# Kernel optimization log

Hardware: AMD Instinct MI355X
Metric: run time of the kernel (lower is better)

## Reference

```python
import jax, jax.numpy as jnp
import numpy as np

EPS = 1e-5

def rmsnorm(x):
    # BitLinear pre-norm (no learnable scale), per BitNet b1.58 reference impl
    return x * jax.lax.rsqrt(jnp.mean(x * x, axis=-1, keepdims=True) + EPS)

def act_quant(x):
    # per-token absmax 8-bit quantization with straight-through estimator
    scale = 127.0 / jnp.clip(jnp.max(jnp.abs(x), axis=-1, keepdims=True), 1e-5)
    q = jnp.clip(jnp.round(x * scale), -128.0, 127.0) / scale
    return x + jax.lax.stop_gradient(q - x)

def weight_quant(w):
    # absmean ternary quantization {-1,0,1} with STE
    scale = 1.0 / jnp.clip(jnp.mean(jnp.abs(w)), 1e-5)
    q = jnp.clip(jnp.round(w * scale), -1.0, 1.0) / scale
    return w + jax.lax.stop_gradient(q - w)

def bitlinear(x, w, b):
    # x: [b, s, d_in], w: [d_out, d_in] (torch Linear layout), b: [d_out]
    xq = act_quant(rmsnorm(x))
    wq = weight_quant(w)
    return jnp.einsum('bsd,fd->bsf', xq, wq) + b

def setup_inputs() -> dict:
    key = jax.random.key(0)
    k0, k1, k2 = jax.random.split(key, 3)
    B, S, D, F = 2, 8192, 1024, 4096  # inner_dim = dim * mult = 4096
    x = jax.random.normal(k0, (B, S, D), dtype=jnp.float32)
    w1 = jax.random.normal(k1, (F, D), dtype=jnp.float32) * (1.0 / np.sqrt(D))
    b1 = jnp.zeros((F,), dtype=jnp.float32)
    w2 = jax.random.normal(k2, (D, F), dtype=jnp.float32) * (1.0 / np.sqrt(F))
    b2 = jnp.zeros((D,), dtype=jnp.float32)
    return {"x": x, "w1": w1, "b1": b1, "w2": w2, "b2": b2}

def reference(x, w1, b1, w2, b2):
    h = bitlinear(x, w1, b1)
    h = jax.nn.gelu(h, approximate=False)  # nn.GELU() default is exact
    # post_act_ln=False -> no LayerNorm; dropout p=0.0 -> identity
    return bitlinear(h, w2, b2)
```

## Files before the change

### kernel.cpp

```cpp
#include <hip/hip_runtime.h>
#include <hip/hip_bf16.h>
#include <stdint.h>

typedef int i32x4 __attribute__((ext_vector_type(4)));

__device__ __forceinline__ float blo(unsigned int u) {
  unsigned int v = u << 16; float f; __builtin_memcpy(&f, &v, 4); return f;
}
__device__ __forceinline__ float bhi(unsigned int u) {
  unsigned int v = u & 0xffff0000u; float f; __builtin_memcpy(&f, &v, 4); return f;
}
__device__ __forceinline__ int pack4q(float a, float b, float c, float d, float qm) {
  int i0 = (int)rintf(a * qm) & 255;
  int i1 = (int)rintf(b * qm) & 255;
  int i2 = (int)rintf(c * qm) & 255;
  int i3 = (int)rintf(d * qm) & 255;
  return i0 | (i1 << 8) | (i2 << 16) | (i3 << 24);
}

__device__ __forceinline__ float fast_gelu(float v) {
  float u = v * 0.70710678118654752f;
  float s = fabsf(u);
  float den = fmaf(0.3275911f, s, 1.0f);
  float t;
  asm("v_rcp_f32 %0, %1" : "=v"(t) : "v"(den));
  float p = t * fmaf(t, fmaf(t, fmaf(t, fmaf(t, 1.061405429f, -1.453152027f),
                                     1.421413741f), -0.284496736f), 0.254829592f);
  float e = fmaf(-p, __expf(-u * u), 1.0f);
  float er = copysignf(e, u);
  return 0.5f * v * (1.0f + er);
}

__global__ void k_reduce_abs2(const float* __restrict__ w1, const float* __restrict__ w2,
                              long n4, float* __restrict__ partials) {
  const int half = gridDim.x >> 1;
  const float* w = (blockIdx.x < half) ? w1 : w2;
  int b = (blockIdx.x < half) ? blockIdx.x : blockIdx.x - half;
  const float4* wv = (const float4*)w;
  float s = 0.0f;
  long stride = (long)half * blockDim.x;
  for (long i = (long)b * blockDim.x + threadIdx.x; i < n4; i += stride) {
    float4 v = wv[i];
    s += fabsf(v.x) + fabsf(v.y) + fabsf(v.z) + fabsf(v.w);
  }
  #pragma unroll
  for (int off = 32; off; off >>= 1) s += __shfl_down(s, off);
  __shared__ float sw[4];
  if ((threadIdx.x & 63) == 0) sw[threadIdx.x >> 6] = s;
  __syncthreads();
  if (threadIdx.x == 0) partials[blockIdx.x] = sw[0] + sw[1] + sw[2] + sw[3];
}

__global__ void k_finalize_scales(const float* __restrict__ p1, const float* __restrict__ p2,
                                  float* __restrict__ scales, float inv1, float inv2) {
  int t = threadIdx.x;
  float s1 = p1[t], s2 = p2[t];
  #pragma unroll
  for (int off = 32; off; off >>= 1) { s1 += __shfl_down(s1, off); s2 += __shfl_down(s2, off); }
  __shared__ float a1[4], a2[4];
  if ((t & 63) == 0) { a1[t >> 6] = s1; a2[t >> 6] = s2; }
  __syncthreads();
  if (t == 0) {
    scales[0] = fmaxf((a1[0]+a1[1]+a1[2]+a1[3]) * inv1, 1e-5f);
    scales[1] = fmaxf((a2[0]+a2[1]+a2[2]+a2[3]) * inv2, 1e-5f);
  }
}

__global__ void k_quant_w2(const float* __restrict__ w1, char* __restrict__ wq1,
                           const float* __restrict__ w2, char* __restrict__ wq2,
                           long n4, const float* __restrict__ scales) {
  const int half = gridDim.x >> 1;
  const bool first = blockIdx.x < half;
  const float* w = first ? w1 : w2;
  char* wq = first ? wq1 : wq2;
  int b = first ? blockIdx.x : blockIdx.x - half;
  float s = 1.0f / scales[first ? 0 : 1];
  const float4* wv = (const float4*)w;
  int* qv = (int*)wq;
  long stride = (long)half * blockDim.x;
  for (long i = (long)b * blockDim.x + threadIdx.x; i < n4; i += stride) {
    float4 v = wv[i];
    int b0 = (int)fminf(fmaxf(rintf(v.x * s), -1.0f), 1.0f) & 255;
    int b1 = (int)fminf(fmaxf(rintf(v.y * s), -1.0f), 1.0f) & 255;
    int b2 = (int)fminf(fmaxf(rintf(v.z * s), -1.0f), 1.0f) & 255;
    int b3 = (int)fminf(fmaxf(rintf(v.w * s), -1.0f), 1.0f) & 255;
    qv[i] = b0 | (b1 << 8) | (b2 << 16) | (b3 << 24);
  }
}

__global__ void k_actq_x(const float* __restrict__ x, char* __restrict__ xq,
                         float* __restrict__ alpha) {
  const int D = 1024;
  size_t t = blockIdx.x;
  int tid = threadIdx.x;
  const float4* row = (const float4*)(x + t * (size_t)D);
  float4 v = row[tid];
  float ss = v.x*v.x + v.y*v.y + v.z*v.z + v.w*v.w;
  float am = fmaxf(fmaxf(fabsf(v.x), fabsf(v.y)), fmaxf(fabsf(v.z), fabsf(v.w)));
  #pragma unroll
  for (int off = 32; off; off >>= 1) {
    ss += __shfl_down(ss, off);
    am = fmaxf(am, __shfl_down(am, off));
  }
  __shared__ float s_ss[4], s_am[4];
  if ((tid & 63) == 0) { s_ss[tid >> 6] = ss; s_am[tid >> 6] = am; }
  __syncthreads();
  ss = s_ss[0] + s_ss[1] + s_ss[2] + s_ss[3];
  am = fmaxf(fmaxf(s_am[0], s_am[1]), fmaxf(s_am[2], s_am[3]));
  float rms = rsqrtf(ss * (1.0f / D) + 1e-5f);
  float a   = fmaxf(am * rms, 1e-5f);
  float qs  = 127.0f / a;
  if (tid == 0) alpha[t] = a * (1.0f / 127.0f);
  int b0 = (int)fminf(fmaxf(rintf((v.x * rms) * qs), -128.0f), 127.0f) & 255;
  int b1 = (int)fminf(fmaxf(rintf((v.y * rms) * qs), -128.0f), 127.0f) & 255;
  int b2 = (int)fminf(fmaxf(rintf((v.z * rms) * qs), -128.0f), 127.0f) & 255;
  int b3 = (int)fminf(fmaxf(rintf((v.w * rms) * qs), -128.0f), 127.0f) & 255;
  ((int*)xq)[t * 256 + tid] = b0 | (b1 << 8) | (b2 << 16) | (b3 << 24);
}

__global__ void k_actq_h(__hip_bfloat16* __restrict__ h, float* __restrict__ alpha) {
  const int F = 4096;
  size_t t = blockIdx.x;
  int tid = threadIdx.x;
  char* rb = (char*)(h + t * (size_t)F);
  const uint4* row = (const uint4*)rb;
  uint4 u0 = row[tid], u1 = row[tid + 256];
  unsigned int uu[8] = {u0.x, u0.y, u0.z, u0.w, u1.x, u1.y, u1.z, u1.w};
  float ss = 0.0f, am = 0.0f;
  #pragma unroll
  for (int i = 0; i < 8; i++) {
    float f0 = blo(uu[i]), f1 = bhi(uu[i]);
    ss += f0 * f0 + f1 * f1;
    am = fmaxf(am, fmaxf(fabsf(f0), fabsf(f1)));
  }
  #pragma unroll
  for (int off = 32; off; off >>= 1) {
    ss += __shfl_down(ss, off);
    am = fmaxf(am, __shfl_down(am, off));
  }
  __shared__ float s_ss[4], s_am[4];
  if ((tid & 63) == 0) { s_ss[tid >> 6] = ss; s_am[tid >> 6] = am; }
  __syncthreads();
  ss = s_ss[0] + s_ss[1] + s_ss[2] + s_ss[3];
  am = fmaxf(fmaxf(s_am[0], s_am[1]), fmaxf(s_am[2], s_am[3]));
  float rms = rsqrtf(ss * (1.0f / F) + 1e-5f);
  float a   = fmaxf(am * rms, 1e-5f);
  float qm  = rms * (127.0f / a);
  if (tid == 0) alpha[t] = a * (1.0f / 127.0f);
  uint2 w0, w1;
  w0.x = (unsigned)pack4q(blo(uu[0]), bhi(uu[0]), blo(uu[1]), bhi(uu[1]), qm);
  w0.y = (unsigned)pack4q(blo(uu[2]), bhi(uu[2]), blo(uu[3]), bhi(uu[3]), qm);
  w1.x = (unsigned)pack4q(blo(uu[4]), bhi(uu[4]), blo(uu[5]), bhi(uu[5]), qm);
  w1.y = (unsigned)pack4q(blo(uu[6]), bhi(uu[6]), blo(uu[7]), bhi(uu[7]), qm);
  *(uint2*)(rb + 8 * tid) = w0;
  *(uint2*)(rb + 2048 + 8 * tid) = w1;
}

#define GLD16(GP, LP) __builtin_amdgcn_global_load_lds( \
    (__attribute__((address_space(1))) void*)(GP), \
    (__attribute__((address_space(3))) void*)(LP), 16, 0, 0)
#define VMCNT3 asm volatile("s_waitcnt vmcnt(3)" ::: "memory")
#define VMCNT0 asm volatile("s_waitcnt vmcnt(0)" ::: "memory")
#define LGKM0  do { asm volatile("s_waitcnt lgkmcnt(0)" ::: "memory"); __builtin_amdgcn_sched_barrier(0); } while(0)

template<int EPI>
__global__ __launch_bounds__(512, 4) void k_gemm_i8(
    const char* __restrict__ A, int lda,
    const char* __restrict__ B,
    const float* __restrict__ bias, const float* __restrict__ alpha,
    const float* __restrict__ scales, int which,
    void* __restrict__ Cout, int N, int K, int lgnbx)
{
  __shared__ __align__(16) char lA[3 * 8192];
  __shared__ __align__(16) char lB[3 * 16384];
  const int tid = threadIdx.x, lane = tid & 63, wid = tid >> 6;
  const int wm = wid >> 2, wn = wid & 3;
  const int nwg = gridDim.x, bid = blockIdx.x;
  const int swz = (bid & 7) * (nwg >> 3) + (bid >> 3);
  const int bx = swz & ((1 << lgnbx) - 1), by = swz >> lgnbx;
  const int m0 = by * 128, n0 = bx * 256;
  const int NT = K >> 6;

  const int srow = tid >> 2, slot = tid & 3;
  const int sswz = (slot ^ ((srow >> 1) & 3)) * 16;
  const char* gA0 = A + (size_t)(m0 +       srow) * lda + sswz;
  const char* gB0 = B + (size_t)(n0 +       srow) * K   + sswz;
  const char* gB1 = B + (size_t)(n0 + 128 + srow) * K   + sswz;
  const int ldst = srow * 64 + slot * 16;

  const int lr = lane & 15;
  const int kx = ((lane >> 4) ^ ((lane >> 1) & 3)) * 16;
  const int aoff = (wm * 64 + lr) * 64 + kx;
  const int boff = (wn * 64 + lr) * 64 + kx;

  GLD16(gA0,      lA + ldst);
  GLD16(gB0,      lB + ldst);
  GLD16(gB1,      lB + 8192 + ldst);
  GLD16(gA0 + 64, lA + 8192 + ldst);
  GLD16(gB0 + 64, lB + 16384 + ldst);
  GLD16(gB1 + 64, lB + 16384 + 8192 + ldst);

  i32x4 acc[4][4] = {};
  int cur = 0, nx1 = 1, nx2 = 2;
  for (int t = 0; t < NT; ++t) {
    if (t + 1 < NT) { VMCNT3; } else { VMCNT0; }
    __builtin_amdgcn_s_barrier();
    if (t + 2 < NT) {
      GLD16(gA0 + 64 * (t + 2), lA + nx2 * 8192 + ldst);
      GLD16(gB0 + 64 * (t + 2), lB + nx2 * 16384 + ldst);
      GLD16(gB1 + 64 * (t + 2), lB + nx2 * 16384 + 8192 + ldst);
    }
    i32x4 av[4], bv[4];
    {
      const char* pa = lA + cur * 8192 + aoff;
      const char* pb = lB + cur * 16384 + boff;
      #pragma unroll
      for (int j = 0; j < 4; ++j) av[j] = *(const i32x4*)(pa + j * 1024);
      #pragma unroll
      for (int n = 0; n < 4; ++n) bv[n] = *(const i32x4*)(pb + n * 1024);
    }
    LGKM0;
    __builtin_amdgcn_s_setprio(1);
    #pragma unroll
    for (int j = 0; j < 4; ++j)
      #pragma unroll
      for (int n = 0; n < 4; ++n)
        acc[j][n] = __builtin_amdgcn_mfma_i32_16x16x64_i8(av[j], bv[n], acc[j][n], 0, 0, 0);
    __builtin_amdgcn_s_setprio(0);
    int tmp = cur; cur = nx1; nx1 = nx2; nx2 = tmp;
  }

  const float wdq = scales[which];
  const int lq4 = (lane >> 4) * 4;
  #pragma unroll
  for (int m = 0; m < 4; ++m) {
    const int rowb = m0 + wm * 64 + m * 16 + lq4;
    float al[4];
    #pragma unroll
    for (int q = 0; q < 4; ++q) al[q] = alpha[rowb + q] * wdq;
    #pragma unroll
    for (int n = 0; n < 4; ++n) {
      const int col = n0 + wn * 64 + n * 16 + lr;
      const float bb = bias[col];
      #pragma unroll
      for (int q = 0; q < 4; ++q) {
        float v = (float)acc[m][n][q] * al[q] + bb;
        if constexpr (EPI == 0) {
          ((__hip_bfloat16*)Cout)[(size_t)(rowb + q) * N + col] = __float2bfloat16(fast_gelu(v));
        } else {
          ((float*)Cout)[(size_t)(rowb + q) * N + col] = v;
        }
      }
    }
  }
}

extern "C" void kernel_launch(void* const* d_in, const int* in_sizes, int n_in,
                              void* d_out, int out_size, void* d_ws, size_t ws_size,
                              hipStream_t stream) {
  const float* x  = (const float*)d_in[0];
  const float* w1 = (const float*)d_in[1];
  const float* b1 = (const float*)d_in[2];
  const float* w2 = (const float*)d_in[3];
  const float* b2 = (const float*)d_in[4];
  const int  F = in_sizes[2];
  const int  D = in_sizes[4];
  const long T = (long)in_sizes[0] / D;
  const long nW = (long)F * D;

  char* ws = (char*)d_ws;
  float* partials = (float*)ws;
  float* scales   = partials + 512;
  float* alpha1 = (float*)(ws + 4096);
  float* alpha2 = alpha1 + T;
  size_t off = 4096 + 2 * (size_t)T * sizeof(float);
  off = (off + 255) & ~(size_t)255;
  char* w1q = ws + off; off += (size_t)nW;
  char* w2q = ws + off; off += (size_t)nW;
  char* xq  = ws + off; off += (size_t)T * D;
  off = (off + 255) & ~(size_t)255;
  __hip_bfloat16* h = (__hip_bfloat16*)(ws + off); off += (size_t)T * F * 2;
  if (ws_size < off) return;

  float invW = (float)(1.0 / (double)nW);
  k_reduce_abs2<<<512, 256, 0, stream>>>(w1, w2, nW / 4, partials);
  k_finalize_scales<<<1, 256, 0, stream>>>(partials, partials + 256, scales, invW, invW);
  k_quant_w2<<<4096, 256, 0, stream>>>(w1, w1q, w2, w2q, nW / 4, scales);
  k_actq_x<<<(unsigned)T, 256, 0, stream>>>(x, xq, alpha1);

  dim3 g1((unsigned)((T / 128) * (F / 256)));
  k_gemm_i8<0><<<g1, 512, 0, stream>>>(xq, D, w1q, b1, alpha1, scales, 0,
                                       h, F, D, __builtin_ctz(F / 256));

  k_actq_h<<<(unsigned)T, 256, 0, stream>>>(h, alpha2);

  dim3 g2((unsigned)((T / 128) * (D / 256)));
  k_gemm_i8<1><<<g2, 512, 0, stream>>>((const char*)h, F * 2, w2q, b2, alpha2, scales, 1,
                                       (float*)d_out, D, F, __builtin_ctz(D / 256));
}
```

Baseline: 244.4 us.

## Use 4-wave GEMM blocks with 64x128 per-wave tiles

The int8 GEMM block shrinks from 512 to 256 threads (4 waves in a 2x2 grid) while keeping the 128x256 block tile. Each wave now computes a 64x128 subtile with 32 accumulators, and each thread issues six global-to-LDS loads per stage instead of three, with the wait count adjusted to match. The aim is more MFMA work per LDS read and fewer waves contending for the barrier. In exchange it raises VGPR pressure and lowers occupancy (launch bounds go to 256 threads with 2 blocks per SM).

Result: slower. 257.7 us (+5.4%).

```diff
diff --git a/kernel.cpp b/kernel.cpp
--- a/kernel.cpp
+++ b/kernel.cpp
@@ -159,12 +159,12 @@
 #define GLD16(GP, LP) __builtin_amdgcn_global_load_lds( \
     (__attribute__((address_space(1))) void*)(GP), \
     (__attribute__((address_space(3))) void*)(LP), 16, 0, 0)
-#define VMCNT3 asm volatile("s_waitcnt vmcnt(3)" ::: "memory")
+#define VMCNT6 asm volatile("s_waitcnt vmcnt(6)" ::: "memory")
 #define VMCNT0 asm volatile("s_waitcnt vmcnt(0)" ::: "memory")
 #define LGKM0  do { asm volatile("s_waitcnt lgkmcnt(0)" ::: "memory"); __builtin_amdgcn_sched_barrier(0); } while(0)
 
 template<int EPI>
-__global__ __launch_bounds__(512, 4) void k_gemm_i8(
+__global__ __launch_bounds__(256, 2) void k_gemm_i8(
     const char* __restrict__ A, int lda,
     const char* __restrict__ B,
     const float* __restrict__ bias, const float* __restrict__ alpha,
@@ -174,7 +174,7 @@
   __shared__ __align__(16) char lA[3 * 8192];
   __shared__ __align__(16) char lB[3 * 16384];
   const int tid = threadIdx.x, lane = tid & 63, wid = tid >> 6;
-  const int wm = wid >> 2, wn = wid & 3;
+  const int wm = wid >> 1, wn = wid & 1;
   const int nwg = gridDim.x, bid = blockIdx.x;
   const int swz = (bid & 7) * (nwg >> 3) + (bid >> 3);
   const int bx = swz & ((1 << lgnbx) - 1), by = swz >> lgnbx;
@@ -183,52 +183,54 @@
 
   const int srow = tid >> 2, slot = tid & 3;
   const int sswz = (slot ^ ((srow >> 1) & 3)) * 16;
-  const char* gA0 = A + (size_t)(m0 +       srow) * lda + sswz;
-  const char* gB0 = B + (size_t)(n0 +       srow) * K   + sswz;
-  const char* gB1 = B + (size_t)(n0 + 128 + srow) * K   + sswz;
+  const char* gA = A + (size_t)(m0 + srow) * lda + sswz;
+  const char* gB = B + (size_t)(n0 + srow) * K + sswz;
+  const size_t ldaj = (size_t)64 * lda, ldbj = (size_t)64 * K;
   const int ldst = srow * 64 + slot * 16;
+
+  #define STAGE(T, BUF) do { \
+    GLD16(gA + 64 * (T),            lA + (BUF) * 8192 + ldst); \
+    GLD16(gA + 64 * (T) + ldaj,     lA + (BUF) * 8192 + 4096 + ldst); \
+    GLD16(gB + 64 * (T),            lB + (BUF) * 16384 + ldst); \
+    GLD16(gB + 64 * (T) + ldbj,     lB + (BUF) * 16384 + 4096 + ldst); \
+    GLD16(gB + 64 * (T) + 2 * ldbj, lB + (BUF) * 16384 + 8192 + ldst); \
+    GLD16(gB + 64 * (T) + 3 * ldbj, lB + (BUF) * 16384 + 12288 + ldst); \
+  } while (0)
 
   const int lr = lane & 15;
   const int kx = ((lane >> 4) ^ ((lane >> 1) & 3)) * 16;
   const int aoff = (wm * 64 + lr) * 64 + kx;
-  const int boff = (wn * 64 + lr) * 64 + kx;
-
-  GLD16(gA0,      lA + ldst);
-  GLD16(gB0,      lB + ldst);
-  GLD16(gB1,      lB + 8192 + ldst);
-  GLD16(gA0 + 64, lA + 8192 + ldst);
-  GLD16(gB0 + 64, lB + 16384 + ldst);
-  GLD16(gB1 + 64, lB + 16384 + 8192 + ldst);
-
-  i32x4 acc[4][4] = {};
+  const int boff = (wn * 128 + lr) * 64 + kx;
+
+  STAGE(0, 0);
+  STAGE(1, 1);
+
+  i32x4 acc[4][8] = {};
   int cur = 0, nx1 = 1, nx2 = 2;
   for (int t = 0; t < NT; ++t) {
-    if (t + 1 < NT) { VMCNT3; } else { VMCNT0; }
+    if (t + 1 < NT) { VMCNT6; } else { VMCNT0; }
     __builtin_amdgcn_s_barrier();
-    if (t + 2 < NT) {
-      GLD16(gA0 + 64 * (t + 2), lA + nx2 * 8192 + ldst);
-      GLD16(gB0 + 64 * (t + 2), lB + nx2 * 16384 + ldst);
-      GLD16(gB1 + 64 * (t + 2), lB + nx2 * 16384 + 8192 + ldst);
-    }
-    i32x4 av[4], bv[4];
+    if (t + 2 < NT) STAGE(t + 2, nx2);
+    i32x4 av[4], bv[8];
     {
       const char* pa = lA + cur * 8192 + aoff;
       const char* pb = lB + cur * 16384 + boff;
       #pragma unroll
       for (int j = 0; j < 4; ++j) av[j] = *(const i32x4*)(pa + j * 1024);
       #pragma unroll
-      for (int n = 0; n < 4; ++n) bv[n] = *(const i32x4*)(pb + n * 1024);
+      for (int n = 0; n < 8; ++n) bv[n] = *(const i32x4*)(pb + n * 1024);
     }
     LGKM0;
     __builtin_amdgcn_s_setprio(1);
     #pragma unroll
     for (int j = 0; j < 4; ++j)
       #pragma unroll
-      for (int n = 0; n < 4; ++n)
+      for (int n = 0; n < 8; ++n)
         acc[j][n] = __builtin_amdgcn_mfma_i32_16x16x64_i8(av[j], bv[n], acc[j][n], 0, 0, 0);
     __builtin_amdgcn_s_setprio(0);
     int tmp = cur; cur = nx1; nx1 = nx2; nx2 = tmp;
   }
+  #undef STAGE
 
   const float wdq = scales[which];
   const int lq4 = (lane >> 4) * 4;
@@ -239,8 +241,8 @@
     #pragma unroll
     for (int q = 0; q < 4; ++q) al[q] = alpha[rowb + q] * wdq;
     #pragma unroll
-    for (int n = 0; n < 4; ++n) {
-      const int col = n0 + wn * 64 + n * 16 + lr;
+    for (int n = 0; n < 8; ++n) {
+      const int col = n0 + wn * 128 + n * 16 + lr;
       const float bb = bias[col];
       #pragma unroll
       for (int q = 0; q < 4; ++q) {
@@ -289,12 +291,12 @@
   k_actq_x<<<(unsigned)T, 256, 0, stream>>>(x, xq, alpha1);
 
   dim3 g1((unsigned)((T / 128) * (F / 256)));
-  k_gemm_i8<0><<<g1, 512, 0, stream>>>(xq, D, w1q, b1, alpha1, scales, 0,
+  k_gemm_i8<0><<<g1, 256, 0, stream>>>(xq, D, w1q, b1, alpha1, scales, 0,
                                        h, F, D, __builtin_ctz(F / 256));
 
   k_actq_h<<<(unsigned)T, 256, 0, stream>>>(h, alpha2);
 
   dim3 g2((unsigned)((T / 128) * (D / 256)));
-  k_gemm_i8<1><<<g2, 512, 0, stream>>>((const char*)h, F * 2, w2q, b2, alpha2, scales, 1,
+  k_gemm_i8<1><<<g2, 256, 0, stream>>>((const char*)h, F * 2, w2q, b2, alpha2, scales, 1,
                                        (float*)d_out, D, F, __builtin_ctz(D / 256));
 }
```

## Split GEMM k-step into two MFMA phases and move GELU into activation quantization

Applied to the files above, without the earlier changes.

The GEMM main loop now splits each k-tile into two halves. Prefetch global-to-LDS loads are spread across them, extra barriers are added, and the A-fragment LDS reads are staggered so MFMA work interleaves with memory issue. GELU is moved out of the first GEMM's epilogue into the activation-quant kernel, so the intermediate bf16 buffer stores pre-GELU values. The aim is to shorten the epilogue and improve overlap, at the cost of extra barriers per iteration and rounding GELU's input to bf16 before applying it.

New measurement: 254.8 us. +4.3%, slower.

```diff
diff --git a/kernel.cpp b/kernel.cpp
--- a/kernel.cpp
+++ b/kernel.cpp
@@ -126,13 +126,15 @@
   const uint4* row = (const uint4*)rb;
   uint4 u0 = row[tid], u1 = row[tid + 256];
   unsigned int uu[8] = {u0.x, u0.y, u0.z, u0.w, u1.x, u1.y, u1.z, u1.w};
+  float f[16];
+  #pragma unroll
+  for (int i = 0; i < 8; i++) {
+    f[2*i]   = fast_gelu(blo(uu[i]));
+    f[2*i+1] = fast_gelu(bhi(uu[i]));
+  }
   float ss = 0.0f, am = 0.0f;
   #pragma unroll
-  for (int i = 0; i < 8; i++) {
-    float f0 = blo(uu[i]), f1 = bhi(uu[i]);
-    ss += f0 * f0 + f1 * f1;
-    am = fmaxf(am, fmaxf(fabsf(f0), fabsf(f1)));
-  }
+  for (int i = 0; i < 16; i++) { ss += f[i] * f[i]; am = fmaxf(am, fabsf(f[i])); }
   #pragma unroll
   for (int off = 32; off; off >>= 1) {
     ss += __shfl_down(ss, off);
@@ -148,10 +150,10 @@
   float qm  = rms * (127.0f / a);
   if (tid == 0) alpha[t] = a * (1.0f / 127.0f);
   uint2 w0, w1;
-  w0.x = (unsigned)pack4q(blo(uu[0]), bhi(uu[0]), blo(uu[1]), bhi(uu[1]), qm);
-  w0.y = (unsigned)pack4q(blo(uu[2]), bhi(uu[2]), blo(uu[3]), bhi(uu[3]), qm);
-  w1.x = (unsigned)pack4q(blo(uu[4]), bhi(uu[4]), blo(uu[5]), bhi(uu[5]), qm);
-  w1.y = (unsigned)pack4q(blo(uu[6]), bhi(uu[6]), blo(uu[7]), bhi(uu[7]), qm);
+  w0.x = (unsigned)pack4q(f[0],  f[1],  f[2],  f[3],  qm);
+  w0.y = (unsigned)pack4q(f[4],  f[5],  f[6],  f[7],  qm);
+  w1.x = (unsigned)pack4q(f[8],  f[9],  f[10], f[11], qm);
+  w1.y = (unsigned)pack4q(f[12], f[13], f[14], f[15], qm);
   *(uint2*)(rb + 8 * tid) = w0;
   *(uint2*)(rb + 2048 + 8 * tid) = w1;
 }
@@ -203,30 +205,45 @@
   i32x4 acc[4][4] = {};
   int cur = 0, nx1 = 1, nx2 = 2;
   for (int t = 0; t < NT; ++t) {
+    const bool pf = (t + 2 < NT);
     if (t + 1 < NT) { VMCNT3; } else { VMCNT0; }
     __builtin_amdgcn_s_barrier();
-    if (t + 2 < NT) {
-      GLD16(gA0 + 64 * (t + 2), lA + nx2 * 8192 + ldst);
-      GLD16(gB0 + 64 * (t + 2), lB + nx2 * 16384 + ldst);
-      GLD16(gB1 + 64 * (t + 2), lB + nx2 * 16384 + 8192 + ldst);
-    }
+    const char* pa = lA + cur * 8192 + aoff;
+    const char* pb = lB + cur * 16384 + boff;
     i32x4 av[4], bv[4];
     {
-      const char* pa = lA + cur * 8192 + aoff;
-      const char* pb = lB + cur * 16384 + boff;
-      #pragma unroll
-      for (int j = 0; j < 4; ++j) av[j] = *(const i32x4*)(pa + j * 1024);
+      av[0] = *(const i32x4*)(pa);
+      av[1] = *(const i32x4*)(pa + 1024);
       #pragma unroll
       for (int n = 0; n < 4; ++n) bv[n] = *(const i32x4*)(pb + n * 1024);
+      if (pf) {
+        GLD16(gA0 + 64 * (t + 2), lA + nx2 * 8192 + ldst);
+        GLD16(gB0 + 64 * (t + 2), lB + nx2 * 16384 + ldst);
+      }
+      __builtin_amdgcn_s_barrier();
+      LGKM0;
+      __builtin_amdgcn_s_setprio(1);
+      #pragma unroll
+      for (int j = 0; j < 2; ++j)
+        #pragma unroll
+        for (int n = 0; n < 4; ++n)
+          acc[j][n] = __builtin_amdgcn_mfma_i32_16x16x64_i8(av[j], bv[n], acc[j][n], 0, 0, 0);
+      __builtin_amdgcn_s_setprio(0);
+      __builtin_amdgcn_s_barrier();
     }
-    LGKM0;
-    __builtin_amdgcn_s_setprio(1);
-    #pragma unroll
-    for (int j = 0; j < 4; ++j)
+    {
+      av[2] = *(const i32x4*)(pa + 2048);
+      av[3] = *(const i32x4*)(pa + 3072);
+      if (pf) GLD16(gB1 + 64 * (t + 2), lB + nx2 * 16384 + 8192 + ldst);
+      LGKM0;
+      __builtin_amdgcn_s_setprio(1);
       #pragma unroll
-      for (int n = 0; n < 4; ++n)
-        acc[j][n] = __builtin_amdgcn_mfma_i32_16x16x64_i8(av[j], bv[n], acc[j][n], 0, 0, 0);
-    __builtin_amdgcn_s_setprio(0);
+      for (int j = 2; j < 4; ++j)
+        #pragma unroll
+        for (int n = 0; n < 4; ++n)
+          acc[j][n] = __builtin_amdgcn_mfma_i32_16x16x64_i8(av[j], bv[n], acc[j][n], 0, 0, 0);
+      __builtin_amdgcn_s_setprio(0);
+    }
     int tmp = cur; cur = nx1; nx1 = nx2; nx2 = tmp;
   }
 
@@ -246,7 +263,7 @@
       for (int q = 0; q < 4; ++q) {
         float v = (float)acc[m][n][q] * al[q] + bb;
         if constexpr (EPI == 0) {
-          ((__hip_bfloat16*)Cout)[(size_t)(rowb + q) * N + col] = __float2bfloat16(fast_gelu(v));
+          ((__hip_bfloat16*)Cout)[(size_t)(rowb + q) * N + col] = __float2bfloat16(v);
         } else {
           ((float*)Cout)[(size_t)(rowb + q) * N + col] = v;
         }
```

## Enlarge int8 GEMM tile to 256x256 with split-phase prefetch; fold scale finalize into quant

Applied to the files above, without the earlier changes.

The int8 GEMM block tile grows from 128x256 to 256x256, so each wave now holds eight M-subtiles of accumulators. Each K-step runs as two MFMA phases with extra barriers, and the A and B prefetches are split between the phases. The aim is to raise arithmetic intensity and cut global and LDS traffic per MFMA, at the cost of more registers (occupancy bound lowered from 4 to 2), more LDS, and fewer workgroups (GEMM2 gets only 256 blocks). Separately, the single-block scale-finalize kernel is removed: every weight-quant block now reduces the partials itself, which saves one launch.

New measurement: 242.9 us. No clear change (-0.6%).

```diff
diff --git a/kernel.cpp b/kernel.cpp
--- a/kernel.cpp
+++ b/kernel.cpp
@@ -51,34 +51,29 @@
   if (threadIdx.x == 0) partials[blockIdx.x] = sw[0] + sw[1] + sw[2] + sw[3];
 }
 
-__global__ void k_finalize_scales(const float* __restrict__ p1, const float* __restrict__ p2,
-                                  float* __restrict__ scales, float inv1, float inv2) {
-  int t = threadIdx.x;
-  float s1 = p1[t], s2 = p2[t];
-  #pragma unroll
-  for (int off = 32; off; off >>= 1) { s1 += __shfl_down(s1, off); s2 += __shfl_down(s2, off); }
-  __shared__ float a1[4], a2[4];
-  if ((t & 63) == 0) { a1[t >> 6] = s1; a2[t >> 6] = s2; }
-  __syncthreads();
-  if (t == 0) {
-    scales[0] = fmaxf((a1[0]+a1[1]+a1[2]+a1[3]) * inv1, 1e-5f);
-    scales[1] = fmaxf((a2[0]+a2[1]+a2[2]+a2[3]) * inv2, 1e-5f);
-  }
-}
-
 __global__ void k_quant_w2(const float* __restrict__ w1, char* __restrict__ wq1,
                            const float* __restrict__ w2, char* __restrict__ wq2,
-                           long n4, const float* __restrict__ scales) {
+                           long n4, const float* __restrict__ partials,
+                           float* __restrict__ scales, float invW) {
   const int half = gridDim.x >> 1;
   const bool first = blockIdx.x < half;
+  int t = threadIdx.x;
+  float p = partials[(first ? 0 : 256) + t];
+  #pragma unroll
+  for (int off = 32; off; off >>= 1) p += __shfl_down(p, off);
+  __shared__ float a[4];
+  if ((t & 63) == 0) a[t >> 6] = p;
+  __syncthreads();
+  float sc = fmaxf((a[0] + a[1] + a[2] + a[3]) * invW, 1e-5f);
+  if (t == 0 && (blockIdx.x == 0 || blockIdx.x == half)) scales[first ? 0 : 1] = sc;
+  float s = 1.0f / sc;
   const float* w = first ? w1 : w2;
   char* wq = first ? wq1 : wq2;
   int b = first ? blockIdx.x : blockIdx.x - half;
-  float s = 1.0f / scales[first ? 0 : 1];
   const float4* wv = (const float4*)w;
   int* qv = (int*)wq;
   long stride = (long)half * blockDim.x;
-  for (long i = (long)b * blockDim.x + threadIdx.x; i < n4; i += stride) {
+  for (long i = (long)b * blockDim.x + t; i < n4; i += stride) {
     float4 v = wv[i];
     int b0 = (int)fminf(fmaxf(rintf(v.x * s), -1.0f), 1.0f) & 255;
     int b1 = (int)fminf(fmaxf(rintf(v.y * s), -1.0f), 1.0f) & 255;
@@ -159,66 +154,68 @@
 #define GLD16(GP, LP) __builtin_amdgcn_global_load_lds( \
     (__attribute__((address_space(1))) void*)(GP), \
     (__attribute__((address_space(3))) void*)(LP), 16, 0, 0)
-#define VMCNT3 asm volatile("s_waitcnt vmcnt(3)" ::: "memory")
+#define VMCNT4 asm volatile("s_waitcnt vmcnt(4)" ::: "memory")
 #define VMCNT0 asm volatile("s_waitcnt vmcnt(0)" ::: "memory")
 #define LGKM0  do { asm volatile("s_waitcnt lgkmcnt(0)" ::: "memory"); __builtin_amdgcn_sched_barrier(0); } while(0)
 
 template<int EPI>
-__global__ __launch_bounds__(512, 4) void k_gemm_i8(
+__global__ __launch_bounds__(512, 2) void k_gemm_i8(
     const char* __restrict__ A, int lda,
     const char* __restrict__ B,
     const float* __restrict__ bias, const float* __restrict__ alpha,
     const float* __restrict__ scales, int which,
     void* __restrict__ Cout, int N, int K, int lgnbx)
 {
-  __shared__ __align__(16) char lA[3 * 8192];
+  __shared__ __align__(16) char lA[3 * 16384];
   __shared__ __align__(16) char lB[3 * 16384];
   const int tid = threadIdx.x, lane = tid & 63, wid = tid >> 6;
   const int wm = wid >> 2, wn = wid & 3;
   const int nwg = gridDim.x, bid = blockIdx.x;
   const int swz = (bid & 7) * (nwg >> 3) + (bid >> 3);
   const int bx = swz & ((1 << lgnbx) - 1), by = swz >> lgnbx;
-  const int m0 = by * 128, n0 = bx * 256;
+  const int m0 = by * 256, n0 = bx * 256;
   const int NT = K >> 6;
 
   const int srow = tid >> 2, slot = tid & 3;
   const int sswz = (slot ^ ((srow >> 1) & 3)) * 16;
   const char* gA0 = A + (size_t)(m0 +       srow) * lda + sswz;
+  const char* gA1 = A + (size_t)(m0 + 128 + srow) * lda + sswz;
   const char* gB0 = B + (size_t)(n0 +       srow) * K   + sswz;
   const char* gB1 = B + (size_t)(n0 + 128 + srow) * K   + sswz;
   const int ldst = srow * 64 + slot * 16;
 
   const int lr = lane & 15;
   const int kx = ((lane >> 4) ^ ((lane >> 1) & 3)) * 16;
-  const int aoff = (wm * 64 + lr) * 64 + kx;
-  const int boff = (wn * 64 + lr) * 64 + kx;
+  const int aoff = (wm * 128 + lr) * 64 + kx;
+  const int boff = (wn * 64  + lr) * 64 + kx;
 
   GLD16(gA0,      lA + ldst);
+  GLD16(gA1,      lA + 8192 + ldst);
   GLD16(gB0,      lB + ldst);
   GLD16(gB1,      lB + 8192 + ldst);
-  GLD16(gA0 + 64, lA + 8192 + ldst);
+  GLD16(gA0 + 64, lA + 16384 + ldst);
+  GLD16(gA1 + 64, lA + 16384 + 8192 + ldst);
   GLD16(gB0 + 64, lB + 16384 + ldst);
   GLD16(gB1 + 64, lB + 16384 + 8192 + ldst);
 
-  i32x4 acc[4][4] = {};
+  i32x4 acc[8][4] = {};
   int cur = 0, nx1 = 1, nx2 = 2;
   for (int t = 0; t < NT; ++t) {
-    if (t + 1 < NT) { VMCNT3; } else { VMCNT0; }
+    const bool pf = (t + 2 < NT);
+    if (t + 1 < NT) { VMCNT4; } else { VMCNT0; }
     __builtin_amdgcn_s_barrier();
-    if (t + 2 < NT) {
-      GLD16(gA0 + 64 * (t + 2), lA + nx2 * 8192 + ldst);
-      GLD16(gB0 + 64 * (t + 2), lB + nx2 * 16384 + ldst);
-      GLD16(gB1 + 64 * (t + 2), lB + nx2 * 16384 + 8192 + ldst);
+    const char* pa = lA + cur * 16384 + aoff;
+    const char* pb = lB + cur * 16384 + boff;
+    i32x4 av[4], bv[4];
+    #pragma unroll
+    for (int j = 0; j < 4; ++j) av[j] = *(const i32x4*)(pa + j * 1024);
+    #pragma unroll
+    for (int n = 0; n < 4; ++n) bv[n] = *(const i32x4*)(pb + n * 1024);
+    if (pf) {
+      GLD16(gA0 + 64 * (t + 2), lA + nx2 * 16384 + ldst);
+      GLD16(gA1 + 64 * (t + 2), lA + nx2 * 16384 + 8192 + ldst);
     }
-    i32x4 av[4], bv[4];
-    {
-      const char* pa = lA + cur * 8192 + aoff;
-      const char* pb = lB + cur * 16384 + boff;
-      #pragma unroll
-      for (int j = 0; j < 4; ++j) av[j] = *(const i32x4*)(pa + j * 1024);
-      #pragma unroll
-      for (int n = 0; n < 4; ++n) bv[n] = *(const i32x4*)(pb + n * 1024);
-    }
+    __builtin_amdgcn_s_barrier();
     LGKM0;
     __builtin_amdgcn_s_setprio(1);
     #pragma unroll
@@ -227,14 +224,29 @@
       for (int n = 0; n < 4; ++n)
         acc[j][n] = __builtin_amdgcn_mfma_i32_16x16x64_i8(av[j], bv[n], acc[j][n], 0, 0, 0);
     __builtin_amdgcn_s_setprio(0);
+    __builtin_amdgcn_s_barrier();
+    #pragma unroll
+    for (int j = 0; j < 4; ++j) av[j] = *(const i32x4*)(pa + (4 + j) * 1024);
+    if (pf) {
+      GLD16(gB0 + 64 * (t + 2), lB + nx2 * 16384 + ldst);
+      GLD16(gB1 + 64 * (t + 2), lB + nx2 * 16384 + 8192 + ldst);
+    }
+    LGKM0;
+    __builtin_amdgcn_s_setprio(1);
+    #pragma unroll
+    for (int j = 0; j < 4; ++j)
+      #pragma unroll
+      for (int n = 0; n < 4; ++n)
+        acc[4 + j][n] = __builtin_amdgcn_mfma_i32_16x16x64_i8(av[j], bv[n], acc[4 + j][n], 0, 0, 0);
+    __builtin_amdgcn_s_setprio(0);
     int tmp = cur; cur = nx1; nx1 = nx2; nx2 = tmp;
   }
 
   const float wdq = scales[which];
   const int lq4 = (lane >> 4) * 4;
   #pragma unroll
-  for (int m = 0; m < 4; ++m) {
-    const int rowb = m0 + wm * 64 + m * 16 + lq4;
+  for (int m = 0; m < 8; ++m) {
+    const int rowb = m0 + wm * 128 + m * 16 + lq4;
     float al[4];
     #pragma unroll
     for (int q = 0; q < 4; ++q) al[q] = alpha[rowb + q] * wdq;
@@ -284,17 +296,16 @@
 
   float invW = (float)(1.0 / (double)nW);
   k_reduce_abs2<<<512, 256, 0, stream>>>(w1, w2, nW / 4, partials);
-  k_finalize_scales<<<1, 256, 0, stream>>>(partials, partials + 256, scales, invW, invW);
-  k_quant_w2<<<4096, 256, 0, stream>>>(w1, w1q, w2, w2q, nW / 4, scales);
+  k_quant_w2<<<4096, 256, 0, stream>>>(w1, w1q, w2, w2q, nW / 4, partials, scales, invW);
   k_actq_x<<<(unsigned)T, 256, 0, stream>>>(x, xq, alpha1);
 
-  dim3 g1((unsigned)((T / 128) * (F / 256)));
+  dim3 g1((unsigned)((T / 256) * (F / 256)));
   k_gemm_i8<0><<<g1, 512, 0, stream>>>(xq, D, w1q, b1, alpha1, scales, 0,
                                        h, F, D, __builtin_ctz(F / 256));
 
   k_actq_h<<<(unsigned)T, 256, 0, stream>>>(h, alpha2);
 
-  dim3 g2((unsigned)((T / 128) * (D / 256)));
+  dim3 g2((unsigned)((T / 256) * (D / 256)));
   k_gemm_i8<1><<<g2, 512, 0, stream>>>((const char*)h, F * 2, w2q, b2, alpha2, scales, 1,
                                        (float*)d_out, D, F, __builtin_ctz(D / 256));
 }
```
